# Kernel tuning notes

Measured on AMD Instinct MI355X. Metric: run time of the kernel, lower is better.

Reference implementation:

```python
import jax, jax.numpy as jnp
import numpy as np

N = 80000      # nodes (spots)
D = 1000       # input_dim (genes)
E = 1280000    # edges (avg degree 16)
FH1, FH2 = 64, 16
GH1, GH2 = 64, 16
K = 10         # dec_cluster_n
ALPHA = 1.0
MASK = int(0.8 * N)
BN_EPS = 1e-3


def _xavier(key, shape):
    fan_in, fan_out = shape[0], shape[1]
    lim = jnp.sqrt(6.0 / (fan_in + fan_out))
    return jax.random.uniform(key, shape, jnp.float32, -lim, lim)


def setup_inputs() -> dict:
    key = jax.random.key(0)
    ks = jax.random.split(key, 32)
    x = jax.random.normal(ks[0], (N, D), jnp.float32)
    edge_rows = jax.random.randint(ks[1], (E,), 0, N, jnp.int32)
    edge_cols = jax.random.randint(ks[2], (E,), 0, N, jnp.int32)
    edge_vals = jax.random.uniform(ks[3], (E,), jnp.float32)
    mask_nodes = jax.random.permutation(ks[4], N)[:MASK].astype(jnp.int32)
    enc_mask_token = 0.02 * jax.random.normal(ks[5], (1, D), jnp.float32)
    # encoder L1: Linear + BatchNorm (eval: running stats)
    W1 = _xavier(ks[6], (D, FH1)); b1 = jnp.zeros((FH1,), jnp.float32)
    g1 = jnp.ones((FH1,), jnp.float32); be1 = jnp.zeros((FH1,), jnp.float32)
    rm1 = 0.1 * jax.random.normal(ks[7], (FH1,), jnp.float32)
    rv1 = 0.5 + jax.random.uniform(ks[8], (FH1,), jnp.float32)
    # encoder L2
    W2 = _xavier(ks[9], (FH1, FH2)); b2 = jnp.zeros((FH2,), jnp.float32)
    g2 = jnp.ones((FH2,), jnp.float32); be2 = jnp.zeros((FH2,), jnp.float32)
    rm2 = 0.1 * jax.random.normal(ks[10], (FH2,), jnp.float32)
    rv2 = 0.5 + jax.random.uniform(ks[11], (FH2,), jnp.float32)
    # GCN weights
    Wgc1 = _xavier(ks[12], (FH2, GH1))
    Wgc2 = _xavier(ks[13], (GH1, GH2))
    Wgc3 = _xavier(ks[14], (GH1, GH2))
    Wdec = _xavier(ks[15], (GH2 + FH2, D))
    cluster_layer = jax.random.normal(ks[16], (K, GH2 + FH2), jnp.float32) * jnp.sqrt(2.0 / (K + GH2 + FH2))
    return dict(x=x, edge_rows=edge_rows, edge_cols=edge_cols, edge_vals=edge_vals,
                mask_nodes=mask_nodes, enc_mask_token=enc_mask_token,
                W1=W1, b1=b1, g1=g1, be1=be1, rm1=rm1, rv1=rv1,
                W2=W2, b2=b2, g2=g2, be2=be2, rm2=rm2, rv2=rv2,
                Wgc1=Wgc1, Wgc2=Wgc2, Wgc3=Wgc3, Wdec=Wdec,
                cluster_layer=cluster_layer)


def _bn_eval(h, g, b, rm, rv):
    return (h - rm) * (g * jax.lax.rsqrt(rv + BN_EPS)) + b


def _spmm(rows, cols, vals, dense):
    # sparse adj [N,N] @ dense [N,F]
    return jax.ops.segment_sum(vals[:, None] * dense[cols], rows, num_segments=N)


def _l2norm(v):
    n = jnp.sqrt(jnp.sum(v * v, axis=-1, keepdims=True))
    return v / jnp.maximum(n, 1e-12)


def reference(x, edge_rows, edge_cols, edge_vals, mask_nodes, enc_mask_token,
              W1, b1, g1, be1, rm1, rv1, W2, b2, g2, be2, rm2, rv2,
              Wgc1, Wgc2, Wgc3, Wdec, cluster_layer):
    # encoding_mask_noise: add mask token to masked nodes (eval: dropout off)
    out_x = x.at[mask_nodes].add(enc_mask_token[0])
    # dense encoder (Linear -> BN(eval) -> ELU; dropout off)
    h = jax.nn.elu(_bn_eval(out_x @ W1 + b1, g1, be1, rm1, rv1))
    feat_x = jax.nn.elu(_bn_eval(h @ W2 + b2, g2, be2, rm2, rv2))
    # GCN layers: mm then spmm
    hidden1 = jax.nn.relu(_spmm(edge_rows, edge_cols, edge_vals, feat_x @ Wgc1))
    mu = _spmm(edge_rows, edge_cols, edge_vals, hidden1 @ Wgc2)
    logvar = _spmm(edge_rows, edge_cols, edge_vals, hidden1 @ Wgc3)
    gnn_z = mu  # eval-mode reparameterize
    z = jnp.concatenate([feat_x, gnn_z], axis=1)  # [N, 32]
    de_feat = _spmm(edge_rows, edge_cols, edge_vals, z @ Wdec)  # identity act
    # student-t cluster soft assignments
    d2 = jnp.sum(jnp.square(z[:, None, :] - cluster_layer[None, :, :]), axis=2)  # [N,K]
    q = 1.0 / (1.0 + d2 / ALPHA)
    q = q ** ((ALPHA + 1.0) / 2.0)
    q = q / jnp.sum(q, axis=1, keepdims=True)
    # sce loss on masked nodes
    x_init = out_x[mask_nodes]
    x_rec = de_feat[mask_nodes]
    loss = jnp.mean((1.0 - jnp.sum(_l2norm(x_rec) * _l2norm(x_init), axis=-1)) ** 3)
    return (z, mu, logvar, de_feat, q, feat_x, gnn_z, loss)
```

## Files before the change

kernel.cpp:

```cpp
#include <hip/hip_runtime.h>
#include <hip/hip_bf16.h>
#include <math.h>

#define Nn 80000
#define Dd 1000
#define Ee 1280000
#define MM 64000
#define NT 32

typedef __attribute__((ext_vector_type(8))) short bf16x8;
typedef __attribute__((ext_vector_type(4))) float f32x4;

__device__ inline unsigned short f2bf(float f){
  union { float f; unsigned u; } c; c.f = f;
  unsigned u = c.u;
  u += 0x7FFFu + ((u >> 16) & 1u);
  return (unsigned short)(u >> 16);
}
__device__ inline float bf2f(unsigned short s){
  return __uint_as_float(((unsigned)s) << 16);
}

__device__ __forceinline__ void gload16(const void* g, void* l){
  __builtin_amdgcn_global_load_lds(
      (const __attribute__((address_space(1))) void*)g,
      (__attribute__((address_space(3))) void*)l, 16, 0, 0);
}

__device__ __forceinline__ bf16x8 cvt8(f32x4 a, f32x4 b){
  union { __hip_bfloat162 h; unsigned u; } c0, c1, c2, c3;
  c0.h = __float22bfloat162_rn(make_float2(a.x, a.y));
  c1.h = __float22bfloat162_rn(make_float2(a.z, a.w));
  c2.h = __float22bfloat162_rn(make_float2(b.x, b.y));
  c3.h = __float22bfloat162_rn(make_float2(b.z, b.w));
  union { unsigned u[4]; bf16x8 v; } r;
  r.u[0] = c0.u; r.u[1] = c1.u; r.u[2] = c2.u; r.u[3] = c3.u;
  return r.v;
}

__global__ __launch_bounds__(256) void k_init(const float* __restrict__ W1,
    const float* __restrict__ Wdec, const float* __restrict__ token,
    unsigned short* __restrict__ Wim, unsigned short* __restrict__ WdT2,
    float* __restrict__ tw, int* __restrict__ flags, int* __restrict__ deg,
    float* __restrict__ loss)
{
  int i = blockIdx.x*256 + threadIdx.x;
  if (i < 131072){
    int t   = i >> 12;
    int rem = i & 4095;
    int c   = rem >> 5;
    int pos = rem & 31;
    int slot = pos >> 3;
    int j    = pos & 7;
    int u    = slot ^ (c & 3);
    int k    = t*32 + u*8 + j;
    float v = 0.f;
    if (c < 96 && k < Dd) v = (c < 64) ? W1[k*64 + c] : Wdec[(size_t)(c-64)*Dd + k];
    Wim[i] = f2bf(v);
  }
  unsigned t1 = (unsigned)(i - 131072);
  if (t1 < 32768u){
    int col = t1 >> 5, k = t1 & 31;
    WdT2[t1] = (col < Dd) ? f2bf(Wdec[(size_t)k*Dd + col]) : (unsigned short)0;
  }
  if (i < Nn){ flags[i] = 0; deg[i] = 0; }
  if (i == 0) *loss = 0.f;
  unsigned u3 = (unsigned)(i - 163840);
  if (u3 < 6208u){
    int j = u3 >> 6, l = u3 & 63;
    float s = 0.f;
    if (j < 64){ for (int k = l; k < Dd; k += 64) s += token[k]*W1[k*64 + j]; }
    else if (j < 96){ const float* wr = Wdec + (size_t)(j-64)*Dd;
                      for (int k = l; k < Dd; k += 64) s += token[k]*wr[k]; }
    else { for (int k = l; k < Dd; k += 64) s += token[k]*token[k]; }
    #pragma unroll
    for (int o = 32; o; o >>= 1) s += __shfl_down(s, o);
    if (l == 0) tw[j] = s;
  }
}

__global__ __launch_bounds__(256) void k_fillb(const int* __restrict__ rows,
    const int* __restrict__ cols, const float* __restrict__ vals,
    const int* __restrict__ mask, int* __restrict__ flags,
    int* __restrict__ deg, int2* __restrict__ buck)
{
  int i = blockIdx.x*256 + threadIdx.x;
  if (i < MM) flags[mask[i]] = 1;
  if (i < Ee){
    int r = rows[i];
    int s = atomicAdd(&deg[r], 1);
    if (s < 64){
      int2 pr; pr.x = cols[i]; pr.y = __float_as_int(vals[i]);
      buck[((size_t)r << 6) + s] = pr;
    }
  }
}

__global__ __launch_bounds__(256, 3) void k_gemm1(
    const float* __restrict__ x, const unsigned short* __restrict__ Wim,
    const int* __restrict__ flags, const float* __restrict__ tw,
    const float* __restrict__ token,
    const float* __restrict__ b1, const float* __restrict__ g1,
    const float* __restrict__ be1, const float* __restrict__ rm1,
    const float* __restrict__ rv1, const float* __restrict__ W2,
    const float* __restrict__ b2, const float* __restrict__ g2,
    const float* __restrict__ be2, const float* __restrict__ rm2,
    const float* __restrict__ rv2, float* __restrict__ fx,
    float* __restrict__ wx, float* __restrict__ sii_node)
{
  __shared__ char smem[53248];
  float* tokL = (float*)(smem + 49152);
  const int tid  = threadIdx.x;
  const int lane = tid & 63;
  const int wave = tid >> 6;
  const int wm = wave >> 1, wn = wave & 1;
  const int l15 = lane & 15, kg = lane >> 4;
  const int swz = l15 & 7;
  const int row0 = blockIdx.x * 128;

  for (int i = tid; i < 1024; i += 256) tokL[i] = (i < Dd) ? token[i] : 0.f;
  __syncthreads();

  auto stage = [&](int t, char* Ab, char* Bb){
    int k0 = t*32;
    #pragma unroll
    for (int j = 0; j < 4; ++j){
      int s = (wave*4 + j)*64 + lane;
      int r = s >> 3, u = s & 7;
      int col = k0 + ((u ^ (r & 7)) << 2);
      if (col > 996) col = 996;
      gload16(x + (size_t)(row0 + r)*Dd + col, Ab + (wave*4 + j)*1024);
    }
    const char* wim = (const char*)Wim + (size_t)t*8192;
    #pragma unroll
    for (int j = 0; j < 2; ++j){
      int ch = wave*2 + j;
      gload16(wim + ch*1024 + lane*16, Bb + ch*1024);
    }
  };

  stage(0, smem,         smem + 32768);
  stage(1, smem + 16384, smem + 40960);

  const f32x4 zero4 = {0.f,0.f,0.f,0.f};
  f32x4 acc[4][3];
  #pragma unroll
  for (int i = 0; i < 4; ++i){ acc[i][0]=zero4; acc[i][1]=zero4; acc[i][2]=zero4; }
  float sx2[4] = {0.f,0.f,0.f,0.f};
  float sxt[4] = {0.f,0.f,0.f,0.f};

  #pragma unroll 2
  for (int t = 0; t < NT; ++t){
    if (t < NT-1) asm volatile("s_waitcnt vmcnt(6)" ::: "memory");
    else          asm volatile("s_waitcnt vmcnt(0)" ::: "memory");
    __builtin_amdgcn_s_barrier();
    __builtin_amdgcn_sched_barrier(0);

    const char* Ab = smem + (t&1)*16384;
    const char* Bb = smem + 32768 + (t&1)*8192;
    const int k0 = t*32;

    f32x4 tk0 = *(const f32x4*)(tokL + k0 + kg*8);
    f32x4 tk1 = *(const f32x4*)(tokL + k0 + kg*8 + 4);

    bf16x8 bfr[3];
    #pragma unroll
    for (int ni = 0; ni < 3; ++ni){
      int c = wn*48 + ni*16 + l15;
      bfr[ni] = *(const bf16x8*)(Bb + c*64 + ((kg ^ (c & 3)) << 4));
    }
    bool kv = (k0 + kg*8) <= 992;
    #pragma unroll
    for (int mi = 0; mi < 4; ++mi){
      int r = wm*64 + mi*16 + l15;
      f32x4 xa = *(const f32x4*)(Ab + r*128 + (((2*kg  ) ^ swz) << 4));
      f32x4 xb = *(const f32x4*)(Ab + r*128 + (((2*kg+1) ^ swz) << 4));
      if (wn == 0 && kv){
        sx2[mi] += xa.x*xa.x + xa.y*xa.y + xa.z*xa.z + xa.w*xa.w
                 + xb.x*xb.x + xb.y*xb.y + xb.z*xb.z + xb.w*xb.w;
        sxt[mi] += xa.x*tk0.x + xa.y*tk0.y + xa.z*tk0.z + xa.w*tk0.w
                 + xb.x*tk1.x + xb.y*tk1.y + xb.z*tk1.z + xb.w*tk1.w;
      }
      bf16x8 af = cvt8(xa, xb);
      acc[mi][0] = __builtin_amdgcn_mfma_f32_16x16x32_bf16(af, bfr[0], acc[mi][0], 0, 0, 0);
      acc[mi][1] = __builtin_amdgcn_mfma_f32_16x16x32_bf16(af, bfr[1], acc[mi][1], 0, 0, 0);
      acc[mi][2] = __builtin_amdgcn_mfma_f32_16x16x32_bf16(af, bfr[2], acc[mi][2], 0, 0, 0);
    }

    __builtin_amdgcn_sched_barrier(0);
    __builtin_amdgcn_s_barrier();
    if (t + 2 < NT)
      stage(t+2, smem + (t&1)*16384, smem + 32768 + (t&1)*8192);
  }

  float stt = tw[96];
  if (wn == 0){
    #pragma unroll
    for (int mi = 0; mi < 4; ++mi){
      float a2 = sx2[mi]; a2 += __shfl_xor(a2, 16); a2 += __shfl_xor(a2, 32);
      float at = sxt[mi]; at += __shfl_xor(at, 16); at += __shfl_xor(at, 32);
      if (lane < 16){
        int row = row0 + wm*64 + mi*16 + lane;
        float fl = flags[row] ? 1.f : 0.f;
        sii_node[row] = a2 + fl*(2.f*at + stt);
      }
    }
  }

  float flv[4][4];
  #pragma unroll
  for (int mi = 0; mi < 4; ++mi)
    #pragma unroll
    for (int r4 = 0; r4 < 4; ++r4)
      flv[mi][r4] = flags[row0 + wm*64 + mi*16 + (lane>>4)*4 + r4] ? 1.f : 0.f;

  float* Hs  = (float*)smem;
  float* W2s = (float*)(smem + 36864);
  for (int i = tid; i < 1024; i += 256) W2s[i] = W2[i];

  #pragma unroll
  for (int ni = 0; ni < 3; ++ni){
    int n = wn*48 + ni*16 + l15;
    float twn = tw[n];
    if (n < 64){
      float bb = b1[n], rmv = rm1[n];
      float scv = g1[n]*rsqrtf(rv1[n] + 1e-3f), bev = be1[n];
      #pragma unroll
      for (int mi = 0; mi < 4; ++mi){
        #pragma unroll
        for (int r4 = 0; r4 < 4; ++r4){
          int lrow = wm*64 + mi*16 + (lane>>4)*4 + r4;
          float v = (acc[mi][ni][r4] + flv[mi][r4]*twn + bb - rmv)*scv + bev;
          v = (v > 0.f) ? v : expm1f(v);
          Hs[lrow*66 + n] = v;
        }
      }
    } else {
      int j = n - 64;
      #pragma unroll
      for (int mi = 0; mi < 4; ++mi){
        #pragma unroll
        for (int r4 = 0; r4 < 4; ++r4){
          int lrow = wm*64 + mi*16 + (lane>>4)*4 + r4;
          wx[(size_t)(row0 + lrow)*32 + j] = acc[mi][ni][r4] + flv[mi][r4]*twn;
        }
      }
    }
  }
  __syncthreads();

  {
    int j = tid & 15;
    float pb = b2[j], prm = rm2[j];
    float psc = g2[j]*rsqrtf(rv2[j] + 1e-3f), pbe = be2[j];
    int rb = (tid >> 4) * 8;
    #pragma unroll
    for (int rr = 0; rr < 8; ++rr){
      int r = rb + rr;
      float a = pb;
      #pragma unroll
      for (int k = 0; k < 64; ++k) a += Hs[r*66 + k]*W2s[k*16 + j];
      float v = (a - prm)*psc + pbe;
      v = (v > 0.f) ? v : expm1f(v);
      fx[(size_t)(row0 + r)*16 + j] = v;
    }
  }
}

template<bool WITH_H1>
__global__ __launch_bounds__(256) void k_spmm16(const int* __restrict__ deg,
    const int2* __restrict__ buck, const float* __restrict__ in,
    float* __restrict__ out, const float* __restrict__ Wgc1,
    unsigned short* __restrict__ h1b)
{
  __shared__ float Ws[1024];
  if (WITH_H1){
    for (int t = threadIdx.x; t < 1024; t += 256) Ws[t] = Wgc1[t];
    __syncthreads();
  }
  int row = blockIdx.x*16 + (threadIdx.x >> 4);
  int l = threadIdx.x & 15;
  int d = deg[row]; if (d > 64) d = 64;
  const int2* bp = buck + ((size_t)row << 6);
  float acc = 0.f;
  for (int p = 0; p < d; ++p){
    int2 ce = bp[p];
    acc += __int_as_float(ce.y) * in[(size_t)ce.x*16 + l];
  }
  out[(size_t)row*16 + l] = acc;
  if (WITH_H1){
    float h0=0.f, h1=0.f, h2=0.f, h3=0.f;
    #pragma unroll
    for (int k = 0; k < 16; ++k){
      float av = __shfl(acc, k, 16);
      const float* wp = &Ws[k*64 + l*4];
      h0 += av*wp[0]; h1 += av*wp[1]; h2 += av*wp[2]; h3 += av*wp[3];
    }
    ushort4 pk;
    pk.x = f2bf(fmaxf(h0, 0.f)); pk.y = f2bf(fmaxf(h1, 0.f));
    pk.z = f2bf(fmaxf(h2, 0.f)); pk.w = f2bf(fmaxf(h3, 0.f));
    *reinterpret_cast<ushort4*>(&h1b[(size_t)row*64 + l*4]) = pk;
  }
}

__global__ __launch_bounds__(256) void k_gcn2(const int* __restrict__ deg,
    const int2* __restrict__ buck, const unsigned short* __restrict__ h1b,
    const float* __restrict__ Wgc2, const float* __restrict__ Wgc3,
    const float* __restrict__ fx, const float* __restrict__ cl,
    float* __restrict__ z, float* __restrict__ mu,
    float* __restrict__ lv, float* __restrict__ gz, float* __restrict__ q)
{
  __shared__ float ah[16][65];
  __shared__ float Ws[2048];
  __shared__ float cls[320];
  __shared__ float zs[16][33];
  __shared__ float qv[16][10];
  int t = threadIdx.x;
  for (int i = t; i < 1024; i += 256){ Ws[i] = Wgc2[i]; Ws[1024 + i] = Wgc3[i]; }
  for (int i = t; i < 320; i += 256) cls[i] = cl[i];
  const int wave = t >> 6, lane = t & 63;
  const int row0 = blockIdx.x*16;
  #pragma unroll
  for (int rr = 0; rr < 4; ++rr){
    int lr = wave*4 + rr;
    int row = row0 + lr;
    int d = deg[row]; if (d > 64) d = 64;
    const int2* bp = buck + ((size_t)row << 6);
    float acc = 0.f;
    for (int p = 0; p < d; ++p){
      int2 ce = bp[p];
      acc += __int_as_float(ce.y) * bf2f(h1b[(size_t)ce.x*64 + lane]);
    }
    ah[lr][lane] = acc;
  }
  __syncthreads();
  {
    int r = t >> 4, j = t & 15;
    const float* ar = ah[r];
    float m = 0.f, l = 0.f;
    #pragma unroll 16
    for (int k = 0; k < 64; ++k){
      float a = ar[k];
      m += a*Ws[k*16 + j];
      l += a*Ws[1024 + k*16 + j];
    }
    size_t grow = (size_t)(row0 + r);
    mu[grow*16 + j] = m;
    gz[grow*16 + j] = m;
    z[grow*32 + 16 + j] = m;
    zs[r][16 + j] = m;
    lv[grow*16 + j] = l;
    float v = fx[grow*16 + j];
    z[grow*32 + j] = v;
    zs[r][j] = v;
  }
  __syncthreads();
  if (t < 160){
    int r = t / 10, c = t - r*10;
    float d2 = 0.f;
    #pragma unroll
    for (int k = 0; k < 32; ++k){ float d = zs[r][k] - cls[c*32 + k]; d2 += d*d; }
    qv[r][c] = 1.f/(1.f + d2);
  }
  __syncthreads();
  if (t < 160){
    int r = t / 10, c = t - r*10;
    float ss = 0.f;
    #pragma unroll
    for (int cc = 0; cc < 10; ++cc) ss += qv[r][cc];
    q[(size_t)(row0 + r)*10 + c] = qv[r][c]/ss;
  }
}

__global__ __launch_bounds__(256) void k_dec(const float* __restrict__ afx,
    const float* __restrict__ amu, const unsigned short* __restrict__ WdT2,
    const float* __restrict__ wx, const float* __restrict__ sii_node,
    float* __restrict__ de, float* __restrict__ term_node)
{
  __shared__ float stg[4][16][68];
  const int lane = threadIdx.x & 63;
  const int wave = threadIdx.x >> 6;
  const int r0 = blockIdx.x*64 + wave*16;
  const int kg = lane >> 4;
  const int l15 = lane & 15;
  const int row = r0 + l15;
  const float* asrc = (kg < 2) ? (afx + (size_t)row*16 + kg*8)
                               : (amu + (size_t)row*16 + (kg-2)*8);
  f32x4 a0 = *reinterpret_cast<const f32x4*>(asrc);
  f32x4 a1 = *reinterpret_cast<const f32x4*>(asrc + 4);
  bf16x8 af = cvt8(a0, a1);
  const float* wsrc = wx + (size_t)row*32 + kg*8;
  f32x4 w0 = *reinterpret_cast<const f32x4*>(wsrc);
  f32x4 w1 = *reinterpret_cast<const f32x4*>(wsrc + 4);
  float sri = a0.x*w0.x + a0.y*w0.y + a0.z*w0.z + a0.w*w0.w
            + a1.x*w1.x + a1.y*w1.y + a1.z*w1.z + a1.w*w1.w;

  const f32x4 zero4 = {0.f,0.f,0.f,0.f};
  float sq = 0.f;
  float (*S)[68] = stg[wave];
  const int srow = lane >> 4;
  const int scol = l15*4;

  for (int g = 0; g < 16; ++g){
    int c0 = g*64;
    #pragma unroll
    for (int j = 0; j < 4; ++j){
      int cb = c0 + j*16;
      bf16x8 bf = *reinterpret_cast<const bf16x8*>(&WdT2[(size_t)(cb + l15)*32 + kg*8]);
      f32x4 d = __builtin_amdgcn_mfma_f32_16x16x32_bf16(bf, af, zero4, 0, 0, 0);
      sq += d[0]*d[0] + d[1]*d[1] + d[2]*d[2] + d[3]*d[3];
      *reinterpret_cast<f32x4*>(&S[l15][j*16 + kg*4]) = d;
    }
    asm volatile("s_waitcnt lgkmcnt(0)" ::: "memory");
    __builtin_amdgcn_sched_barrier(0);
    #pragma unroll
    for (int sub = 0; sub < 4; ++sub){
      int lr = sub*4 + srow;
      int cc = c0 + scol;
      if (cc < Dd){
        f32x4 v = *reinterpret_cast<const f32x4*>(&S[lr][scol]);
        *reinterpret_cast<f32x4*>(&de[(size_t)(r0 + lr)*Dd + cc]) = v;
      }
    }
    __builtin_amdgcn_sched_barrier(0);
    asm volatile("s_waitcnt lgkmcnt(0)" ::: "memory");
  }
  sq  += __shfl_xor(sq, 16);  sq  += __shfl_xor(sq, 32);
  sri += __shfl_xor(sri, 16); sri += __shfl_xor(sri, 32);
  if (kg == 0){
    float nr = fmaxf(sqrtf(sq), 1e-12f);
    float ni = fmaxf(sqrtf(sii_node[row]), 1e-12f);
    float tt = 1.f - sri/(nr*ni);
    term_node[row] = tt*tt*tt;
  }
}

__global__ __launch_bounds__(256) void k_lossred(const float* __restrict__ term_node,
    const int* __restrict__ mask, float* __restrict__ loss)
{
  int i = blockIdx.x*256 + threadIdx.x;
  float s = 0.f;
  for (int w = i; w < MM; w += 64*256) s += term_node[mask[w]];
  #pragma unroll
  for (int o = 32; o; o >>= 1) s += __shfl_down(s, o);
  __shared__ float red[4];
  if ((threadIdx.x & 63) == 0) red[threadIdx.x >> 6] = s;
  __syncthreads();
  if (threadIdx.x == 0)
    atomicAdd(loss, (red[0] + red[1] + red[2] + red[3]) * (1.f/MM));
}

extern "C" void kernel_launch(void* const* d_in, const int* in_sizes, int n_in,
                              void* d_out, int out_size, void* d_ws, size_t ws_size,
                              hipStream_t stream)
{
  const float* x     = (const float*)d_in[0];
  const int*   erow  = (const int*)  d_in[1];
  const int*   ecol  = (const int*)  d_in[2];
  const float* evls  = (const float*)d_in[3];
  const int*   mask  = (const int*)  d_in[4];
  const float* token = (const float*)d_in[5];
  const float* W1  = (const float*)d_in[6];
  const float* b1  = (const float*)d_in[7];
  const float* g1  = (const float*)d_in[8];
  const float* be1 = (const float*)d_in[9];
  const float* rm1 = (const float*)d_in[10];
  const float* rv1 = (const float*)d_in[11];
  const float* W2  = (const float*)d_in[12];
  const float* b2  = (const float*)d_in[13];
  const float* g2  = (const float*)d_in[14];
  const float* be2 = (const float*)d_in[15];
  const float* rm2 = (const float*)d_in[16];
  const float* rv2 = (const float*)d_in[17];
  const float* Wgc1= (const float*)d_in[18];
  const float* Wgc2= (const float*)d_in[19];
  const float* Wgc3= (const float*)d_in[20];
  const float* Wdec= (const float*)d_in[21];
  const float* clus= (const float*)d_in[22];

  float* out = (float*)d_out;
  float* oz  = out;
  float* omu = out + (size_t)Nn*32;
  float* olv = omu + (size_t)Nn*16;
  float* ode = olv + (size_t)Nn*16;
  float* oq  = ode + (size_t)Nn*1000;
  float* ofx = oq  + (size_t)Nn*10;
  float* ogz = ofx + (size_t)Nn*16;
  float* olo = ogz + (size_t)Nn*16;

  char* w = (char*)d_ws;
  unsigned short* Wim  = (unsigned short*)w; w += (size_t)262144;
  unsigned short* WdT2 = (unsigned short*)w; w += (size_t)65536;
  float* tw    = (float*)w; w += 512;
  int* flags   = (int*)w;   w += (size_t)Nn*4;
  int* deg     = (int*)w;   w += (size_t)Nn*4;
  int2* buck   = (int2*)w;  w += (size_t)Nn*64*8;
  float* afx   = (float*)w; w += (size_t)Nn*16*4;
  float* amu   = (float*)w; w += (size_t)Nn*16*4;
  unsigned short* h1b = (unsigned short*)w; w += (size_t)Nn*64*2;
  float* wx    = (float*)w; w += (size_t)Nn*32*4;
  float* sii   = (float*)w; w += (size_t)Nn*4;
  float* term  = (float*)w; w += (size_t)Nn*4;

  k_init<<<dim3(665), dim3(256), 0, stream>>>(W1, Wdec, token, Wim, WdT2, tw,
      flags, deg, olo);
  k_fillb<<<dim3((Ee+255)/256), dim3(256), 0, stream>>>(erow, ecol, evls, mask,
      flags, deg, buck);
  k_gemm1<<<dim3(Nn/128), dim3(256), 0, stream>>>(x, Wim, flags, tw, token,
      b1, g1, be1, rm1, rv1, W2, b2, g2, be2, rm2, rv2, ofx, wx, sii);
  k_spmm16<true><<<dim3(Nn/16), dim3(256), 0, stream>>>(deg, buck, ofx, afx, Wgc1, h1b);
  k_gcn2<<<dim3(Nn/16), dim3(256), 0, stream>>>(deg, buck, h1b, Wgc2, Wgc3,
      ofx, clus, oz, omu, olv, ogz, oq);
  k_spmm16<false><<<dim3(Nn/16), dim3(256), 0, stream>>>(deg, buck, omu, amu, nullptr, nullptr);
  k_dec<<<dim3(Nn/64), dim3(256), 0, stream>>>(afx, amu, WdT2, wx, sii, ode, term);
  k_lossred<<<dim3(64), dim3(256), 0, stream>>>(term, mask, olo);
}
```

Baseline: 550.5 us.

## Split edge bucketing into two row-range passes and fuse loss reduction into decoder

The edge bucketing kernel now runs twice, each pass handling only edges whose row falls in one half of the node range. This is meant to concentrate atomic and scatter traffic on a smaller region per pass, at the cost of reading the full row array twice. The separate loss-reduction kernel is removed: the decoder multiplies each row's term by the mask flag, reduces within the block and atomically adds into the loss. This saves a launch and the per-node term buffer, but adds one atomic per decoder block.

```diff
diff --git a/kernel.cpp b/kernel.cpp
--- a/kernel.cpp
+++ b/kernel.cpp
@@ -82,16 +82,18 @@
 __global__ __launch_bounds__(256) void k_fillb(const int* __restrict__ rows,
     const int* __restrict__ cols, const float* __restrict__ vals,
     const int* __restrict__ mask, int* __restrict__ flags,
-    int* __restrict__ deg, int2* __restrict__ buck)
+    int* __restrict__ deg, int2* __restrict__ buck, int lo, int hi)
 {
   int i = blockIdx.x*256 + threadIdx.x;
-  if (i < MM) flags[mask[i]] = 1;
+  if (lo == 0 && i < MM) flags[mask[i]] = 1;
   if (i < Ee){
     int r = rows[i];
-    int s = atomicAdd(&deg[r], 1);
-    if (s < 64){
-      int2 pr; pr.x = cols[i]; pr.y = __float_as_int(vals[i]);
-      buck[((size_t)r << 6) + s] = pr;
+    if (r >= lo && r < hi){
+      int s = atomicAdd(&deg[r], 1);
+      if (s < 64){
+        int2 pr; pr.x = cols[i]; pr.y = __float_as_int(vals[i]);
+        buck[((size_t)r << 6) + s] = pr;
+      }
     }
   }
 }
@@ -375,9 +377,11 @@
 __global__ __launch_bounds__(256) void k_dec(const float* __restrict__ afx,
     const float* __restrict__ amu, const unsigned short* __restrict__ WdT2,
     const float* __restrict__ wx, const float* __restrict__ sii_node,
-    float* __restrict__ de, float* __restrict__ term_node)
+    const int* __restrict__ flags, float* __restrict__ de,
+    float* __restrict__ loss)
 {
   __shared__ float stg[4][16][68];
+  __shared__ float bsum[4];
   const int lane = threadIdx.x & 63;
   const int wave = threadIdx.x >> 6;
   const int r0 = blockIdx.x*64 + wave*16;
@@ -427,27 +431,19 @@
   }
   sq  += __shfl_xor(sq, 16);  sq  += __shfl_xor(sq, 32);
   sri += __shfl_xor(sri, 16); sri += __shfl_xor(sri, 32);
+  float tval = 0.f;
   if (kg == 0){
     float nr = fmaxf(sqrtf(sq), 1e-12f);
     float ni = fmaxf(sqrtf(sii_node[row]), 1e-12f);
     float tt = 1.f - sri/(nr*ni);
-    term_node[row] = tt*tt*tt;
-  }
-}
-
-__global__ __launch_bounds__(256) void k_lossred(const float* __restrict__ term_node,
-    const int* __restrict__ mask, float* __restrict__ loss)
-{
-  int i = blockIdx.x*256 + threadIdx.x;
-  float s = 0.f;
-  for (int w = i; w < MM; w += 64*256) s += term_node[mask[w]];
+    tval = flags[row] ? tt*tt*tt : 0.f;
+  }
   #pragma unroll
-  for (int o = 32; o; o >>= 1) s += __shfl_down(s, o);
-  __shared__ float red[4];
-  if ((threadIdx.x & 63) == 0) red[threadIdx.x >> 6] = s;
+  for (int o = 1; o < 16; o <<= 1) tval += __shfl_xor(tval, o);
+  if (lane == 0) bsum[wave] = tval;
   __syncthreads();
   if (threadIdx.x == 0)
-    atomicAdd(loss, (red[0] + red[1] + red[2] + red[3]) * (1.f/MM));
+    atomicAdd(loss, (bsum[0] + bsum[1] + bsum[2] + bsum[3]) * (1.f/MM));
 }
 
 extern "C" void kernel_launch(void* const* d_in, const int* in_sizes, int n_in,
@@ -500,18 +496,18 @@
   unsigned short* h1b = (unsigned short*)w; w += (size_t)Nn*64*2;
   float* wx    = (float*)w; w += (size_t)Nn*32*4;
   float* sii   = (float*)w; w += (size_t)Nn*4;
-  float* term  = (float*)w; w += (size_t)Nn*4;
 
   k_init<<<dim3(665), dim3(256), 0, stream>>>(W1, Wdec, token, Wim, WdT2, tw,
       flags, deg, olo);
   k_fillb<<<dim3((Ee+255)/256), dim3(256), 0, stream>>>(erow, ecol, evls, mask,
-      flags, deg, buck);
+      flags, deg, buck, 0, 40000);
+  k_fillb<<<dim3((Ee+255)/256), dim3(256), 0, stream>>>(erow, ecol, evls, mask,
+      flags, deg, buck, 40000, 80000);
   k_gemm1<<<dim3(Nn/128), dim3(256), 0, stream>>>(x, Wim, flags, tw, token,
       b1, g1, be1, rm1, rv1, W2, b2, g2, be2, rm2, rv2, ofx, wx, sii);
   k_spmm16<true><<<dim3(Nn/16), dim3(256), 0, stream>>>(deg, buck, ofx, afx, Wgc1, h1b);
   k_gcn2<<<dim3(Nn/16), dim3(256), 0, stream>>>(deg, buck, h1b, Wgc2, Wgc3,
       ofx, clus, oz, omu, olv, ogz, oq);
   k_spmm16<false><<<dim3(Nn/16), dim3(256), 0, stream>>>(deg, buck, omu, amu, nullptr, nullptr);
-  k_dec<<<dim3(Nn/64), dim3(256), 0, stream>>>(afx, amu, WdT2, wx, sii, ode, term);
-  k_lossred<<<dim3(64), dim3(256), 0, stream>>>(term, mask, olo);
-}
+  k_dec<<<dim3(Nn/64), dim3(256), 0, stream>>>(afx, amu, WdT2, wx, sii, flags, ode, olo);
+}
```

Result: no change. 544.3 us (-1.1%).
